# Performance work log

Hardware: AMD Instinct MI355X
Metric: run time of the kernel (lower is better)

The kernel has to match this reference:

```python
import jax, jax.numpy as jnp
import numpy as np

N, E, IN, HID, HEADS, OUT = 50000, 800000, 128, 64, 4, 64


def setup_inputs() -> dict:
    key = jax.random.key(0)
    ks = jax.random.split(key, 13)
    s1 = 1.0 / np.sqrt(IN)
    s2 = 1.0 / np.sqrt(HID * HEADS)
    s3 = 1.0 / np.sqrt(HID)
    return {
        'x': jax.random.normal(ks[0], (N, IN), dtype=jnp.float32),
        'edge_index': jax.random.randint(ks[1], (2, E), 0, N, dtype=jnp.int64),
        # GATv2 layer 1: heads=HEADS, out=HID, concat=True
        'W1l': jax.random.normal(ks[2], (IN, HEADS * HID), dtype=jnp.float32) * s1,
        'W1r': jax.random.normal(ks[3], (IN, HEADS * HID), dtype=jnp.float32) * s1,
        'att1': jax.random.normal(ks[4], (HEADS, HID), dtype=jnp.float32) * s3,
        'b1': jnp.zeros((HEADS * HID,), dtype=jnp.float32),
        # GATv2 layer 2: heads=1, out=HID
        'W2l': jax.random.normal(ks[5], (HEADS * HID, HID), dtype=jnp.float32) * s2,
        'W2r': jax.random.normal(ks[6], (HEADS * HID, HID), dtype=jnp.float32) * s2,
        'att2': jax.random.normal(ks[7], (1, HID), dtype=jnp.float32) * s3,
        'b2': jnp.zeros((HID,), dtype=jnp.float32),
        # final Linear(HID, OUT)
        'Wlin': jax.random.normal(ks[8], (HID, OUT), dtype=jnp.float32) * s3,
        'blin': jnp.zeros((OUT,), dtype=jnp.float32),
    }


def _gatv2(x, src, dst, Wl, Wr, att, bias, n):
    # PyG GATv2Conv (share_weights=False): x_j -> lin_l, x_i -> lin_r
    H, C = att.shape
    xl = (x @ Wl).reshape(n, H, C)  # source transform [N,H,C]
    xr = (x @ Wr).reshape(n, H, C)  # destination transform [N,H,C]
    # per-edge GATv2 score: a^T LeakyReLU(xl_j + xr_i)
    e = jnp.sum(jax.nn.leaky_relu(xl[src] + xr[dst], 0.2) * att, axis=-1)  # [E,H]
    # scatter-softmax over edges sharing a destination
    m = jax.ops.segment_max(e, dst, num_segments=n)  # [N,H]
    ex = jnp.exp(e - m[dst])
    denom = jax.ops.segment_sum(ex, dst, num_segments=n)
    alpha = ex / (denom[dst] + 1e-16)  # [E,H]
    # weighted scatter-add aggregation of source features
    out = jax.ops.segment_sum(xl[src] * alpha[:, :, None], dst, num_segments=n)  # [N,H,C]
    return out.reshape(n, H * C) + bias


def reference(x, edge_index, W1l, W1r, att1, b1, W2l, W2r, att2, b2, Wlin, blin):
    n = x.shape[0]
    loops = jnp.arange(n, dtype=edge_index.dtype)
    src = jnp.concatenate([edge_index[0], loops])  # add_self_loops=True (PyG default)
    dst = jnp.concatenate([edge_index[1], loops])
    h = _gatv2(x, src, dst, W1l, W1r, att1, b1, n)
    h = jax.nn.elu(h)
    h = _gatv2(h, src, dst, W2l, W2r, att2, b2, n)
    h = jax.nn.elu(h)
    return h @ Wlin + blin
```

## Files before the change

### kernel.cpp

```cpp
#include <hip/hip_runtime.h>
#include <hip/hip_bf16.h>
#include <math.h>

#define N_NODES 50000
#define N_EDGES 800000
#define ETOT (N_EDGES + N_NODES)
#define NB_SCAN 196

typedef __attribute__((ext_vector_type(8))) short short8;
typedef __attribute__((ext_vector_type(4))) float floatx4;
typedef __attribute__((ext_vector_type(2))) float f32x2;

__device__ __forceinline__ float bf_lo(unsigned u) { return __uint_as_float(u << 16); }
__device__ __forceinline__ float bf_hi(unsigned u) { return __uint_as_float(u & 0xffff0000u); }
__device__ __forceinline__ unsigned short f2bf(float f) {
    unsigned u = __float_as_uint(f);
    return (unsigned short)((u + 0x7fffu + ((u >> 16) & 1u)) >> 16);
}
__device__ __forceinline__ unsigned pack2bf(float a, float b) {
    return (unsigned)f2bf(a) | ((unsigned)f2bf(b) << 16);
}
#define DPP_ADD(p, ctrl) \
    (p) += __int_as_float(__builtin_amdgcn_update_dpp(0, __float_as_int(p), (ctrl), 0xF, 0xF, true))

__global__ __launch_bounds__(256) void k_prep(const float* __restrict__ W1l,
                                              const float* __restrict__ W1r,
                                              const float* __restrict__ W2l,
                                              const float* __restrict__ W2r,
                                              unsigned short* __restrict__ Wt1,
                                              unsigned short* __restrict__ Wt2,
                                              int* __restrict__ deg) {
    const int b = blockIdx.x;
    if (b < 384) {
        const int idx = b * 256 + threadIdx.x;
        if (idx < 65536) {
            const int k = idx >> 9;
            const int n = idx & 511;
            const float v = (n < 256) ? W1l[k * 256 + n] : W1r[k * 256 + (n - 256)];
            Wt1[n * 128 + k] = f2bf(v);
        } else {
            const int j = idx - 65536;
            const int k = j >> 7;
            const int n = j & 127;
            const float v = (n < 64) ? W2l[k * 64 + n] : W2r[k * 64 + (n - 64)];
            Wt2[n * 256 + k] = f2bf(v);
        }
    } else {
        const int i = (b - 384) * 256 + threadIdx.x;
        if (i < N_NODES) deg[i] = 0;
    }
}

__global__ __launch_bounds__(256) void k_g1h(const float* __restrict__ x,
                                             const unsigned short* __restrict__ Wt1,
                                             unsigned short* __restrict__ xlb,
                                             unsigned short* __restrict__ xrb,
                                             const int* __restrict__ ei,
                                             int* __restrict__ deg) {
    __shared__ unsigned short sA[128 * 136];
    const int b = blockIdx.x;
    if (b >= 782) {
        for (long e = (long)(b - 782) * 256 + threadIdx.x; e < ETOT; e += 1024 * 256) {
            const int d = (e < N_EDGES) ? ei[N_EDGES + e] : (int)(e - N_EDGES);
            atomicAdd(&deg[d], 1);
        }
        return;
    }
    const int t = threadIdx.x;
    const int lane = t & 63, wv = t >> 6;
    const int m0 = (b >> 1) * 128;
    const int flavor = b & 1;
#pragma unroll
    for (int j = 0; j < 16; j++) {
        const int i4 = t + j * 256;
        const int row = i4 >> 5, k4 = i4 & 31;
        float4 v = make_float4(0.f, 0.f, 0.f, 0.f);
        if (m0 + row < N_NODES) v = ((const float4*)x)[(long)(m0 + row) * 32 + k4];
        ushort4 u;
        u.x = f2bf(v.x); u.y = f2bf(v.y); u.z = f2bf(v.z); u.w = f2bf(v.w);
        *(ushort4*)&sA[row * 136 + k4 * 4] = u;
    }
    __syncthreads();
    const int l15 = lane & 15, quad = lane >> 4;
    const int nloc0 = wv * 64;
    unsigned short* outp = flavor ? xrb : xlb;
    short8 bfr[4][4];
#pragma unroll
    for (int nt = 0; nt < 4; nt++)
#pragma unroll
        for (int ks = 0; ks < 4; ks++)
            bfr[nt][ks] = *(const short8*)&Wt1[(flavor * 256 + nloc0 + nt * 16 + l15) * 128 + ks * 32 + quad * 8];
    for (int mt = 0; mt < 8; mt++) {
        short8 a[4];
#pragma unroll
        for (int ks = 0; ks < 4; ks++)
            a[ks] = *(const short8*)&sA[(mt * 16 + l15) * 136 + ks * 32 + quad * 8];
        floatx4 acc[4];
#pragma unroll
        for (int nt = 0; nt < 4; nt++) {
            acc[nt] = (floatx4)(0.f);
#pragma unroll
            for (int ks = 0; ks < 4; ks++)
                acc[nt] = __builtin_amdgcn_mfma_f32_16x16x32_bf16(a[ks], bfr[nt][ks], acc[nt], 0, 0, 0);
        }
        const int mrow0 = m0 + mt * 16 + quad * 4;
#pragma unroll
        for (int nt = 0; nt < 4; nt++) {
            const int n = nloc0 + nt * 16 + l15;
#pragma unroll
            for (int r = 0; r < 4; r++) {
                const int m = mrow0 + r;
                if (m < N_NODES) outp[(long)m * 256 + n] = f2bf(acc[nt][r]);
            }
        }
    }
}

__global__ __launch_bounds__(256) void k_scan1(const int* __restrict__ deg,
                                               int* __restrict__ rowstart,
                                               int* __restrict__ blocksum) {
    __shared__ int wsum[4];
    const int t = threadIdx.x, lane = t & 63, wv = t >> 6;
    const int i = blockIdx.x * 256 + t;
    const int v = (i < N_NODES) ? deg[i] : 0;
    int incl = v;
#pragma unroll
    for (int off = 1; off < 64; off <<= 1) {
        const int u = __shfl_up(incl, off);
        if (lane >= off) incl += u;
    }
    if (lane == 63) wsum[wv] = incl;
    __syncthreads();
    int woff = 0;
#pragma unroll
    for (int j = 0; j < 4; j++) woff += (j < wv) ? wsum[j] : 0;
    const int excl = incl - v + woff;
    if (i < N_NODES) rowstart[i] = excl;
    if (t == 255) blocksum[blockIdx.x] = excl + v;
}

__global__ __launch_bounds__(256) void k_scan2(const int* __restrict__ blocksum,
                                               int* __restrict__ blockoff) {
    __shared__ int wsum[4];
    const int t = threadIdx.x, lane = t & 63, wv = t >> 6;
    const int v = (t < NB_SCAN) ? blocksum[t] : 0;
    int incl = v;
#pragma unroll
    for (int off = 1; off < 64; off <<= 1) {
        const int u = __shfl_up(incl, off);
        if (lane >= off) incl += u;
    }
    if (lane == 63) wsum[wv] = incl;
    __syncthreads();
    int woff = 0;
#pragma unroll
    for (int j = 0; j < 4; j++) woff += (j < wv) ? wsum[j] : 0;
    if (t < NB_SCAN) blockoff[t] = incl - v + woff;
}

__global__ __launch_bounds__(256) void k_scan3(int* __restrict__ rowstart,
                                               const int* __restrict__ blockoff,
                                               int* __restrict__ cursor) {
    const int i = blockIdx.x * 256 + threadIdx.x;
    if (i < N_NODES) {
        const int r = rowstart[i] + blockoff[blockIdx.x];
        rowstart[i] = r;
        cursor[i] = r;
    }
}

__global__ __launch_bounds__(256) void k_scatter(const int* __restrict__ ei,
                                                 int* __restrict__ cursor,
                                                 int* __restrict__ csr) {
    const long e = (long)blockIdx.x * 256 + threadIdx.x;
    if (e >= ETOT) return;
    int s, d;
    if (e < N_EDGES) { s = ei[e]; d = ei[N_EDGES + e]; }
    else { s = d = (int)(e - N_EDGES); }
    const int pos = atomicAdd(&cursor[d], 1);
    csr[pos] = s << 9;
}

__global__ __launch_bounds__(256) void k_node1(const int* __restrict__ rowstart,
                                               const int* __restrict__ deg,
                                               const int* __restrict__ csr,
                                               const uint4* __restrict__ xlb,
                                               const uint4* __restrict__ xrb,
                                               const float* __restrict__ att,
                                               const float* __restrict__ b1,
                                               uint4* __restrict__ h1b) {
    const int lane = threadIdx.x & 63;
    const int wv = threadIdx.x >> 6;
    const int node = blockIdx.x * 4 + wv;
    const int g = lane >> 5;
    const int l = lane & 31;
    const char* xlbase = (const char*)xlb;
    const uint4 xru = xrb[(long)node * 32 + l];
    const float4 ta = ((const float4*)att)[2 * l];
    const float4 tb = ((const float4*)att)[2 * l + 1];
    f32x2 xp[4], tp[4];
    xp[0] = (f32x2){bf_lo(xru.x), bf_hi(xru.x)};
    xp[1] = (f32x2){bf_lo(xru.y), bf_hi(xru.y)};
    xp[2] = (f32x2){bf_lo(xru.z), bf_hi(xru.z)};
    xp[3] = (f32x2){bf_lo(xru.w), bf_hi(xru.w)};
    tp[0] = (f32x2){ta.x, ta.y}; tp[1] = (f32x2){ta.z, ta.w};
    tp[2] = (f32x2){tb.x, tb.y}; tp[3] = (f32x2){tb.z, tb.w};
    const int start = rowstart[node];
    const int cnt = deg[node];
    const int ns = (cnt - g + 1) >> 1;
    float den = 0.f;
    f32x2 acc[4];
#pragma unroll
    for (int c = 0; c < 4; c++) acc[c] = (f32x2)(0.f);

    auto body = [&](const uint4& rr) {
        f32x2 a0, a1, a2, a3;
        a0.x = bf_lo(rr.x); a0.y = bf_hi(rr.x);
        a1.x = bf_lo(rr.y); a1.y = bf_hi(rr.y);
        a2.x = bf_lo(rr.z); a2.y = bf_hi(rr.z);
        a3.x = bf_lo(rr.w); a3.y = bf_hi(rr.w);
        f32x2 v = a0 + xp[0];
        f32x2 p2 = __builtin_elementwise_max(v, v * 0.2f) * tp[0];
        v = a1 + xp[1]; p2 += __builtin_elementwise_max(v, v * 0.2f) * tp[1];
        v = a2 + xp[2]; p2 += __builtin_elementwise_max(v, v * 0.2f) * tp[2];
        v = a3 + xp[3]; p2 += __builtin_elementwise_max(v, v * 0.2f) * tp[3];
        float p = p2.x + p2.y;
        DPP_ADD(p, 0xB1);
        DPP_ADD(p, 0x4E);
        DPP_ADD(p, 0x141);
        const float w = __expf(p);
        acc[0] += a0 * w;
        acc[1] += a1 * w;
        acc[2] += a2 * w;
        acc[3] += a3 * w;
        den += w;
    };

    uint4 rcur = make_uint4(0, 0, 0, 0), rnext = rcur;
    if (ns > 0) rcur = *((const uint4*)(xlbase + csr[start + g]) + l);
    if (ns > 1) rnext = *((const uint4*)(xlbase + csr[start + 2 + g]) + l);
    int i = 0;
    for (; i + 2 < ns; i++) {
        const uint4 r2 = *((const uint4*)(xlbase + csr[start + 2 * (i + 2) + g]) + l);
        body(rcur);
        rcur = rnext; rnext = r2;
    }
    for (; i < ns; i++) {
        body(rcur);
        rcur = rnext;
    }
    den += __shfl_xor(den, 32);
    const float inv = 1.f / (den + 1e-16f);
#pragma unroll
    for (int c = 0; c < 4; c++) {
        f32x2 t2 = acc[c];
        t2.x += __shfl_xor(t2.x, 32);
        t2.y += __shfl_xor(t2.y, 32);
        acc[c] = t2;
    }
    const float4 ba = ((const float4*)b1)[2 * l];
    const float4 bb = ((const float4*)b1)[2 * l + 1];
    f32x2 bp[4];
    bp[0] = (f32x2){ba.x, ba.y}; bp[1] = (f32x2){ba.z, ba.w};
    bp[2] = (f32x2){bb.x, bb.y}; bp[3] = (f32x2){bb.z, bb.w};
    float o[8];
#pragma unroll
    for (int c = 0; c < 4; c++) {
        f32x2 t2 = acc[c] * inv + bp[c];
        o[2 * c]     = t2.x > 0.f ? t2.x : expm1f(t2.x);
        o[2 * c + 1] = t2.y > 0.f ? t2.y : expm1f(t2.y);
    }
    if (g == 0) {
        uint4 u;
        u.x = pack2bf(o[0], o[1]);
        u.y = pack2bf(o[2], o[3]);
        u.z = pack2bf(o[4], o[5]);
        u.w = pack2bf(o[6], o[7]);
        h1b[(long)node * 32 + l] = u;
    }
}

__global__ __launch_bounds__(256) void k_gemm2(const uint4* __restrict__ h,
                                               const unsigned short* __restrict__ Wt2,
                                               unsigned short* __restrict__ xlb,
                                               unsigned short* __restrict__ xrb) {
    __shared__ unsigned short sA[64 * 264];
    const int t = threadIdx.x;
    const int lane = t & 63, wv = t >> 6;
    const int m0 = blockIdx.x * 64;
#pragma unroll
    for (int j = 0; j < 8; j++) {
        const int i8 = t + j * 256;
        const int row = i8 >> 5, c8 = i8 & 31;
        uint4 v = make_uint4(0, 0, 0, 0);
        if (m0 + row < N_NODES) v = h[(long)(m0 + row) * 32 + c8];
        *(uint4*)&sA[row * 264 + c8 * 8] = v;
    }
    __syncthreads();
    const int l15 = lane & 15, quad = lane >> 4;
    const int ncol0 = wv * 32;
    short8 b[2][8];
#pragma unroll
    for (int nt = 0; nt < 2; nt++)
#pragma unroll
        for (int ks = 0; ks < 8; ks++)
            b[nt][ks] = *(const short8*)&Wt2[(ncol0 + nt * 16 + l15) * 256 + ks * 32 + quad * 8];
    for (int mt = 0; mt < 4; mt++) {
        floatx4 acc[2];
        acc[0] = (floatx4)(0.f);
        acc[1] = (floatx4)(0.f);
#pragma unroll
        for (int ks = 0; ks < 8; ks++) {
            const short8 a = *(const short8*)&sA[(mt * 16 + l15) * 264 + ks * 32 + quad * 8];
            acc[0] = __builtin_amdgcn_mfma_f32_16x16x32_bf16(a, b[0][ks], acc[0], 0, 0, 0);
            acc[1] = __builtin_amdgcn_mfma_f32_16x16x32_bf16(a, b[1][ks], acc[1], 0, 0, 0);
        }
        const int mrow0 = m0 + mt * 16 + quad * 4;
#pragma unroll
        for (int nt = 0; nt < 2; nt++) {
            const int n = ncol0 + nt * 16 + l15;
#pragma unroll
            for (int r = 0; r < 4; r++) {
                const int m = mrow0 + r;
                if (m < N_NODES) {
                    if (n < 64) xlb[(long)m * 64 + n] = f2bf(acc[nt][r]);
                    else        xrb[(long)m * 64 + (n - 64)] = f2bf(acc[nt][r]);
                }
            }
        }
    }
}

__global__ __launch_bounds__(256) void k_node2(const int* __restrict__ rowstart,
                                               const int* __restrict__ deg,
                                               const int* __restrict__ csr,
                                               const uint2* __restrict__ xlb,
                                               const uint2* __restrict__ xrb,
                                               const float* __restrict__ att,
                                               const float* __restrict__ b2,
                                               const float* __restrict__ Wlin,
                                               const float* __restrict__ blin,
                                               float* __restrict__ out) {
    __shared__ float sh[4][64];
    const int lane = threadIdx.x & 63;
    const int wv = threadIdx.x >> 6;
    const int node = blockIdx.x * 4 + wv;
    const int g = lane >> 4;
    const int l = lane & 15;
    const char* xlbase = (const char*)xlb;
    const uint2 xru = xrb[(long)node * 16 + l];
    const float4 at4 = ((const float4*)att)[l];
    f32x2 xp[2], tp[2];
    xp[0] = (f32x2){bf_lo(xru.x), bf_hi(xru.x)};
    xp[1] = (f32x2){bf_lo(xru.y), bf_hi(xru.y)};
    tp[0] = (f32x2){at4.x, at4.y}; tp[1] = (f32x2){at4.z, at4.w};
    const int start = rowstart[node];
    const int cnt = deg[node];
    const int ns = (cnt - g + 3) >> 2;
    float den = 0.f;
    f32x2 acc[2];
    acc[0] = (f32x2)(0.f); acc[1] = (f32x2)(0.f);

    auto body = [&](const uint2& rr) {
        f32x2 a0, a1;
        a0.x = bf_lo(rr.x); a0.y = bf_hi(rr.x);
        a1.x = bf_lo(rr.y); a1.y = bf_hi(rr.y);
        f32x2 v = a0 + xp[0];
        f32x2 p2 = __builtin_elementwise_max(v, v * 0.2f) * tp[0];
        v = a1 + xp[1]; p2 += __builtin_elementwise_max(v, v * 0.2f) * tp[1];
        float p = p2.x + p2.y;
        DPP_ADD(p, 0xB1);
        DPP_ADD(p, 0x4E);
        DPP_ADD(p, 0x141);
        DPP_ADD(p, 0x140);
        const float w = __expf(p);
        acc[0] += a0 * w;
        acc[1] += a1 * w;
        den += w;
    };

    uint2 rcur = make_uint2(0, 0), rnext = rcur;
    if (ns > 0) rcur = *((const uint2*)(xlbase + (csr[start + g] >> 2)) + l);
    if (ns > 1) rnext = *((const uint2*)(xlbase + (csr[start + 4 + g] >> 2)) + l);
    int i = 0;
    for (; i + 2 < ns; i++) {
        const uint2 r2 = *((const uint2*)(xlbase + (csr[start + 4 * (i + 2) + g] >> 2)) + l);
        body(rcur);
        rcur = rnext; rnext = r2;
    }
    for (; i < ns; i++) {
        body(rcur);
        rcur = rnext;
    }
    den += __shfl_xor(den, 16);
    den += __shfl_xor(den, 32);
    const float inv = 1.f / (den + 1e-16f);
    float t0 = acc[0].x, t1 = acc[0].y, t2 = acc[1].x, t3 = acc[1].y;
    t0 += __shfl_xor(t0, 16); t0 += __shfl_xor(t0, 32);
    t1 += __shfl_xor(t1, 16); t1 += __shfl_xor(t1, 32);
    t2 += __shfl_xor(t2, 16); t2 += __shfl_xor(t2, 32);
    t3 += __shfl_xor(t3, 16); t3 += __shfl_xor(t3, 32);
    const float4 b4 = ((const float4*)b2)[l];
    float4 h4;
    h4.x = t0 * inv + b4.x; h4.x = h4.x > 0.f ? h4.x : expm1f(h4.x);
    h4.y = t1 * inv + b4.y; h4.y = h4.y > 0.f ? h4.y : expm1f(h4.y);
    h4.z = t2 * inv + b4.z; h4.z = h4.z > 0.f ? h4.z : expm1f(h4.z);
    h4.w = t3 * inv + b4.w; h4.w = h4.w > 0.f ? h4.w : expm1f(h4.w);
    if (g == 0) ((float4*)sh[wv])[l] = h4;
    __syncthreads();
    float o = blin[lane];
#pragma unroll
    for (int k = 0; k < 64; k++) o = fmaf(sh[wv][k], Wlin[k * 64 + lane], o);
    out[(long)node * 64 + lane] = o;
}

extern "C" void kernel_launch(void* const* d_in, const int* in_sizes, int n_in,
                              void* d_out, int out_size, void* d_ws, size_t ws_size,
                              hipStream_t stream) {
    (void)in_sizes; (void)n_in; (void)out_size; (void)ws_size;
    const float* x    = (const float*)d_in[0];
    const int*   ei   = (const int*)d_in[1];
    const float* W1l  = (const float*)d_in[2];
    const float* W1r  = (const float*)d_in[3];
    const float* att1 = (const float*)d_in[4];
    const float* b1   = (const float*)d_in[5];
    const float* W2l  = (const float*)d_in[6];
    const float* W2r  = (const float*)d_in[7];
    const float* att2 = (const float*)d_in[8];
    const float* b2   = (const float*)d_in[9];
    const float* Wlin = (const float*)d_in[10];
    const float* blin = (const float*)d_in[11];

    float* ws = (float*)d_ws;
    unsigned short* XL1b = (unsigned short*)(ws);
    unsigned short* XR1b = (unsigned short*)(ws + 6400000);
    uint4*          H1b  = (uint4*)(ws + 12800000);
    unsigned short* XL2b = (unsigned short*)(ws + 19200000);
    unsigned short* XR2b = (unsigned short*)(ws + 20800000);
    int* deg      = (int*)(ws + 22400000);
    int* rowstart = deg + 50000;
    int* cursor   = rowstart + 50000;
    int* blocksum = cursor + 50000;
    int* blockoff = blocksum + 256;
    int* csr      = blockoff + 256;
    unsigned short* Wt1 = (unsigned short*)(ws + 23500000);
    unsigned short* Wt2 = (unsigned short*)(ws + 23550000);

    k_prep<<<580, 256, 0, stream>>>(W1l, W1r, W2l, W2r, Wt1, Wt2, deg);
    k_g1h<<<1806, 256, 0, stream>>>(x, Wt1, XL1b, XR1b, ei, deg);
    k_scan1<<<NB_SCAN, 256, 0, stream>>>(deg, rowstart, blocksum);
    k_scan2<<<1, 256, 0, stream>>>(blocksum, blockoff);
    k_scan3<<<NB_SCAN, 256, 0, stream>>>(rowstart, blockoff, cursor);
    k_scatter<<<(ETOT + 255) / 256, 256, 0, stream>>>(ei, cursor, csr);
    k_node1<<<12500, 256, 0, stream>>>(rowstart, deg, csr,
                                       (const uint4*)XL1b, (const uint4*)XR1b,
                                       att1, b1, H1b);
    k_gemm2<<<782, 256, 0, stream>>>((const uint4*)H1b, Wt2, XL2b, XR2b);
    k_node2<<<12500, 256, 0, stream>>>(rowstart, deg, csr,
                                       (const uint2*)XL2b, (const uint2*)XR2b,
                                       att2, b2, Wlin, blin, (float*)d_out);
}
```

Baseline: 333.3 us.

## Move final linear layer out of node2 into separate bf16 MFMA GEMM kernel

The final Linear(64,64) is no longer a per-node scalar FMA loop at the end of the layer-2 aggregation kernel. Node2 now writes the ELU output as bf16 to a workspace buffer, and a new kernel applies Wlin using bf16 MFMA 16x16x32 tiles. The prep kernel also produces a transposed bf16 copy of Wlin. This removes 64 dependent FMAs and a block-wide sync from the latency-bound gather kernel. In exchange it adds a kernel launch, an extra round trip through global memory, and bf16 rounding of the hidden activations before the last matmul.

Result: faster. 309.7 us (-7.1%).

```diff
diff --git a/kernel.cpp b/kernel.cpp
--- a/kernel.cpp
+++ b/kernel.cpp
@@ -27,26 +27,32 @@
                                               const float* __restrict__ W1r,
                                               const float* __restrict__ W2l,
                                               const float* __restrict__ W2r,
+                                              const float* __restrict__ Wlin,
                                               unsigned short* __restrict__ Wt1,
                                               unsigned short* __restrict__ Wt2,
+                                              unsigned short* __restrict__ Wt3,
                                               int* __restrict__ deg) {
     const int b = blockIdx.x;
-    if (b < 384) {
+    if (b < 400) {
         const int idx = b * 256 + threadIdx.x;
         if (idx < 65536) {
             const int k = idx >> 9;
             const int n = idx & 511;
             const float v = (n < 256) ? W1l[k * 256 + n] : W1r[k * 256 + (n - 256)];
             Wt1[n * 128 + k] = f2bf(v);
-        } else {
+        } else if (idx < 98304) {
             const int j = idx - 65536;
             const int k = j >> 7;
             const int n = j & 127;
             const float v = (n < 64) ? W2l[k * 64 + n] : W2r[k * 64 + (n - 64)];
             Wt2[n * 256 + k] = f2bf(v);
+        } else {
+            const int j = idx - 98304;
+            const int n = j >> 6, k = j & 63;
+            Wt3[n * 64 + k] = f2bf(Wlin[k * 64 + n]);
         }
     } else {
-        const int i = (b - 384) * 256 + threadIdx.x;
+        const int i = (b - 400) * 256 + threadIdx.x;
         if (i < N_NODES) deg[i] = 0;
     }
 }
@@ -338,10 +344,7 @@
                                                const uint2* __restrict__ xrb,
                                                const float* __restrict__ att,
                                                const float* __restrict__ b2,
-                                               const float* __restrict__ Wlin,
-                                               const float* __restrict__ blin,
-                                               float* __restrict__ out) {
-    __shared__ float sh[4][64];
+                                               uint2* __restrict__ h2b) {
     const int lane = threadIdx.x & 63;
     const int wv = threadIdx.x >> 6;
     const int node = blockIdx.x * 4 + wv;
@@ -406,12 +409,50 @@
     h4.y = t1 * inv + b4.y; h4.y = h4.y > 0.f ? h4.y : expm1f(h4.y);
     h4.z = t2 * inv + b4.z; h4.z = h4.z > 0.f ? h4.z : expm1f(h4.z);
     h4.w = t3 * inv + b4.w; h4.w = h4.w > 0.f ? h4.w : expm1f(h4.w);
-    if (g == 0) ((float4*)sh[wv])[l] = h4;
+    if (g == 0) {
+        uint2 u;
+        u.x = pack2bf(h4.x, h4.y);
+        u.y = pack2bf(h4.z, h4.w);
+        h2b[(long)node * 16 + l] = u;
+    }
+}
+
+__global__ __launch_bounds__(256) void k_gemm3(const uint4* __restrict__ h2,
+                                               const unsigned short* __restrict__ Wt3,
+                                               const float* __restrict__ blin,
+                                               float* __restrict__ out) {
+    __shared__ unsigned short sA[64 * 72];
+    const int t = threadIdx.x;
+    const int lane = t & 63, wv = t >> 6;
+    const int m0 = blockIdx.x * 64;
+#pragma unroll
+    for (int j = 0; j < 2; j++) {
+        const int i8 = t + j * 256;
+        const int row = i8 >> 3, c8 = i8 & 7;
+        uint4 v = make_uint4(0, 0, 0, 0);
+        if (m0 + row < N_NODES) v = h2[(long)(m0 + row) * 8 + c8];
+        *(uint4*)&sA[row * 72 + c8 * 8] = v;
+    }
     __syncthreads();
-    float o = blin[lane];
-#pragma unroll
-    for (int k = 0; k < 64; k++) o = fmaf(sh[wv][k], Wlin[k * 64 + lane], o);
-    out[(long)node * 64 + lane] = o;
+    const int l15 = lane & 15, quad = lane >> 4;
+    const int n0 = wv * 16;
+    const short8 b0 = *(const short8*)&Wt3[(n0 + l15) * 64 + quad * 8];
+    const short8 b1 = *(const short8*)&Wt3[(n0 + l15) * 64 + 32 + quad * 8];
+    const float bl = blin[n0 + l15];
+#pragma unroll
+    for (int mt = 0; mt < 4; mt++) {
+        const short8 a0 = *(const short8*)&sA[(mt * 16 + l15) * 72 + quad * 8];
+        const short8 a1 = *(const short8*)&sA[(mt * 16 + l15) * 72 + 32 + quad * 8];
+        floatx4 acc = (floatx4)(0.f);
+        acc = __builtin_amdgcn_mfma_f32_16x16x32_bf16(a0, b0, acc, 0, 0, 0);
+        acc = __builtin_amdgcn_mfma_f32_16x16x32_bf16(a1, b1, acc, 0, 0, 0);
+        const int mrow0 = m0 + mt * 16 + quad * 4;
+#pragma unroll
+        for (int r = 0; r < 4; r++) {
+            const int m = mrow0 + r;
+            if (m < N_NODES) out[(long)m * 64 + n0 + l15] = acc[r] + bl;
+        }
+    }
 }
 
 extern "C" void kernel_launch(void* const* d_in, const int* in_sizes, int n_in,
@@ -433,6 +474,7 @@
 
     float* ws = (float*)d_ws;
     unsigned short* XL1b = (unsigned short*)(ws);
+    uint2*          H2b  = (uint2*)(ws);
     unsigned short* XR1b = (unsigned short*)(ws + 6400000);
     uint4*          H1b  = (uint4*)(ws + 12800000);
     unsigned short* XL2b = (unsigned short*)(ws + 19200000);
@@ -445,8 +487,9 @@
     int* csr      = blockoff + 256;
     unsigned short* Wt1 = (unsigned short*)(ws + 23500000);
     unsigned short* Wt2 = (unsigned short*)(ws + 23550000);
-
-    k_prep<<<580, 256, 0, stream>>>(W1l, W1r, W2l, W2r, Wt1, Wt2, deg);
+    unsigned short* Wt3 = (unsigned short*)(ws + 23600000);
+
+    k_prep<<<596, 256, 0, stream>>>(W1l, W1r, W2l, W2r, Wlin, Wt1, Wt2, Wt3, deg);
     k_g1h<<<1806, 256, 0, stream>>>(x, Wt1, XL1b, XR1b, ei, deg);
     k_scan1<<<NB_SCAN, 256, 0, stream>>>(deg, rowstart, blocksum);
     k_scan2<<<1, 256, 0, stream>>>(blocksum, blockoff);
@@ -458,5 +501,6 @@
     k_gemm2<<<782, 256, 0, stream>>>((const uint4*)H1b, Wt2, XL2b, XR2b);
     k_node2<<<12500, 256, 0, stream>>>(rowstart, deg, csr,
                                        (const uint2*)XL2b, (const uint2*)XR2b,
-                                       att2, b2, Wlin, blin, (float*)d_out);
-}
+                                       att2, b2, H2b);
+    k_gemm3<<<782, 256, 0, stream>>>((const uint4*)H2b, Wt3, blin, (float*)d_out);
+}
```
